# Kernel optimization log

Measured on AMD Instinct MI355X. Metric: run time of the kernel, lower is better.

Reference implementation:

```python
import jax, jax.numpy as jnp
import numpy as np

N_NODES = 50000
N_EDGES = 1600000
D = 128
N_GRAPHS = 512


def _glorot(key, shape):
    fan_in, fan_out = shape[1], shape[0]
    lim = float(np.sqrt(6.0 / (fan_in + fan_out)))
    return jax.random.uniform(key, shape, jnp.float32, -lim, lim)


def setup_inputs() -> dict:
    key = jax.random.key(0)
    ks = jax.random.split(key, 16)
    inp = {
        "x": jax.random.normal(ks[0], (N_NODES, D), jnp.float32),
        "edge_index": jax.random.randint(ks[1], (2, N_EDGES), 0, N_NODES, jnp.int64),
        "batch": jnp.sort(jax.random.randint(ks[2], (N_NODES,), 0, N_GRAPHS, jnp.int64)),
    }
    # 3 SAGEConv layers: W_l (neighbor path, with bias), W_r (root path, no bias)
    for l in range(3):
        inp[f"Wl{l}"] = _glorot(ks[3 + 3 * l], (D, D))
        inp[f"b{l}"] = jnp.zeros((D,), jnp.float32)
        inp[f"Wr{l}"] = _glorot(ks[4 + 3 * l], (D, D))
    inp["fc_w"] = _glorot(ks[14], (1, D))
    inp["fc_b"] = jnp.zeros((1,), jnp.float32)
    return inp


def _sage_layer(x, src, dst, Wl, b, Wr):
    # mean aggregation of source features at destination nodes
    deg = jax.ops.segment_sum(jnp.ones((src.shape[0],), x.dtype), dst, num_segments=N_NODES)
    agg = jax.ops.segment_sum(x[src], dst, num_segments=N_NODES)  # [N, D] gather+scatter
    agg = agg / jnp.clip(deg, 1.0)[:, None]
    return agg @ Wl.T + b + x @ Wr.T


def reference(x, edge_index, batch, Wl0, b0, Wr0, Wl1, b1, Wr1, Wl2, b2, Wr2, fc_w, fc_b):
    src, dst = edge_index[0], edge_index[1]
    for Wl, b, Wr in ((Wl0, b0, Wr0), (Wl1, b1, Wr1), (Wl2, b2, Wr2)):
        x = jax.nn.relu(_sage_layer(x, src, dst, Wl, b, Wr))  # dropout p=0 -> identity
    # global mean pool per graph
    cnt = jax.ops.segment_sum(jnp.ones((x.shape[0],), x.dtype), batch, num_segments=N_GRAPHS)
    pooled = jax.ops.segment_sum(x, batch, num_segments=N_GRAPHS) / jnp.clip(cnt, 1.0)[:, None]
    return pooled @ fc_w.T + fc_b
```

## Files before the change

### kernel.cpp

```cpp
#include <hip/hip_runtime.h>

#define N_NODES  50000
#define N_EDGES  1600000
#define DIM      128
#define N_GRAPHS 512
#define SCAN_BLOCK 1024
#define NB1   196
#define B1    256
#define CHUNK 6250
#define BH_N  (NB1 * B1)
#define BH_BLK ((BH_N + SCAN_BLOCK - 1) / SCAN_BLOCK)

typedef unsigned int uint_t;
typedef unsigned short ushort_t;
typedef __attribute__((ext_vector_type(8))) short bf16x8;
typedef __attribute__((ext_vector_type(4))) float f32x4;

__device__ inline uint_t bf_rne(float f) {
    uint_t u = __float_as_uint(f);
    return (u + 0x7fffu + ((u >> 16) & 1u)) >> 16;
}

__device__ inline void bf_split(float f, uint_t& h, uint_t& l) {
    h = bf_rne(f);
    float hf = __uint_as_float(h << 16);
    l = bf_rne(f - hf);
}

__global__ __launch_bounds__(256) void p1_count(const int* __restrict__ dst,
                                                int* __restrict__ bh) {
    __shared__ int hist[NB1];
    int b = blockIdx.x, t = threadIdx.x;
    for (int i = t; i < NB1; i += 256) hist[i] = 0;
    __syncthreads();
    int base = b * CHUNK;
    for (int i = t; i < CHUNK; i += 256)
        atomicAdd(&hist[dst[base + i] >> 8], 1);
    __syncthreads();
    for (int i = t; i < NB1; i += 256) bh[i * B1 + b] = hist[i];
}

__global__ void block_reduce_n(const int* __restrict__ in, int* __restrict__ bsum, int n) {
    __shared__ int red[256];
    int b = blockIdx.x, t = threadIdx.x;
    int base = b * SCAN_BLOCK;
    int s = 0;
    for (int i = t; i < SCAN_BLOCK; i += 256) {
        int idx = base + i;
        s += (idx < n) ? in[idx] : 0;
    }
    red[t] = s; __syncthreads();
    for (int off = 128; off; off >>= 1) {
        if (t < off) red[t] += red[t + off];
        __syncthreads();
    }
    if (t == 0) bsum[b] = red[0];
}

__global__ void scan_tops_n(const int* __restrict__ bsum, int* __restrict__ bofs, int nblk) {
    if (threadIdx.x == 0) {
        int acc = 0;
        for (int i = 0; i < nblk; i++) { bofs[i] = acc; acc += bsum[i]; }
    }
}

__global__ void block_scan_n(const int* __restrict__ in, const int* __restrict__ bofs,
                             int* __restrict__ ofs, int n) {
    __shared__ int tmp[SCAN_BLOCK];
    int b = blockIdx.x, t = threadIdx.x;
    int i = b * SCAN_BLOCK + t;
    tmp[t] = (i < n) ? in[i] : 0;
    __syncthreads();
    for (int off = 1; off < SCAN_BLOCK; off <<= 1) {
        int add = (t >= off) ? tmp[t - off] : 0;
        __syncthreads();
        tmp[t] += add;
        __syncthreads();
    }
    if (i < n) ofs[i + 1] = tmp[t] + bofs[b];
    if (i == 0) ofs[0] = 0;
}

__global__ __launch_bounds__(256) void p1_scatter(const int* __restrict__ src,
                                                  const int* __restrict__ dst,
                                                  const int* __restrict__ bhofs,
                                                  uint_t* __restrict__ ebuf1) {
    __shared__ int cur[NB1];
    int b = blockIdx.x, t = threadIdx.x;
    for (int i = t; i < NB1; i += 256) cur[i] = bhofs[i * B1 + b];
    __syncthreads();
    int base = b * CHUNK;
    for (int i = t; i < CHUNK; i += 256) {
        int d = dst[base + i];
        int pos = atomicAdd(&cur[d >> 8], 1);
        ebuf1[pos] = (uint_t)src[base + i] | ((uint_t)(d & 255) << 16);
    }
}

__global__ __launch_bounds__(256) void p2_sort(const uint_t* __restrict__ ebuf1,
                                               const int* __restrict__ bhofs,
                                               int* __restrict__ row_start,
                                               int* __restrict__ ebuf) {
    __shared__ int hist[256];
    __shared__ int scn[256];
    __shared__ int cur[256];
    int k = blockIdx.x, t = threadIdx.x;
    int s = bhofs[k * B1];
    int e = (k == NB1 - 1) ? N_EDGES : bhofs[(k + 1) * B1];
    hist[t] = 0;
    __syncthreads();
    for (int i = s + t; i < e; i += 256)
        atomicAdd(&hist[(ebuf1[i] >> 16) & 255], 1);
    __syncthreads();
    int v = hist[t];
    scn[t] = v;
    __syncthreads();
    for (int off = 1; off < 256; off <<= 1) {
        int add = (t >= off) ? scn[t - off] : 0;
        __syncthreads();
        scn[t] += add;
        __syncthreads();
    }
    int ex = scn[t] - v;
    int node = k * 256 + t;
    if (node < N_NODES) row_start[node] = s + ex;
    if (k == NB1 - 1 && t == 0) row_start[N_NODES] = N_EDGES;
    cur[t] = s + ex;
    __syncthreads();
    for (int i = s + t; i < e; i += 256) {
        uint_t p = ebuf1[i];
        int pos = atomicAdd(&cur[(p >> 16) & 255], 1);
        ebuf[pos] = (int)(p & 0xffffu);
    }
}

__global__ void xsplit(const float* __restrict__ x, ushort_t* __restrict__ xh,
                       ushort_t* __restrict__ xl) {
    int i = blockIdx.x * 256 + threadIdx.x;
    if (i < (N_NODES * DIM) / 4) {
        float4 v = ((const float4*)x)[i];
        uint_t h0,h1,h2,h3,l0,l1,l2,l3;
        bf_split(v.x,h0,l0); bf_split(v.y,h1,l1); bf_split(v.z,h2,l2); bf_split(v.w,h3,l3);
        uint2 ho; ho.x = h0 | (h1 << 16); ho.y = h2 | (h3 << 16);
        uint2 lo; lo.x = l0 | (l1 << 16); lo.y = l2 | (l3 << 16);
        ((uint2*)xh)[i] = ho;
        ((uint2*)xl)[i] = lo;
    }
}

__global__ void wsplit6(const float* w0, const float* w1, const float* w2,
                        const float* w3, const float* w4, const float* w5,
                        ushort_t* __restrict__ whi) {
    int i = blockIdx.x * 256 + threadIdx.x;
    if (i < 6 * 16384) {
        int ws = i >> 14, off = i & 16383;
        const float* w = (ws == 0) ? w0 : (ws == 1) ? w1 : (ws == 2) ? w2
                       : (ws == 3) ? w3 : (ws == 4) ? w4 : w5;
        whi[i] = (ushort_t)bf_rne(w[off]);
    }
}

__global__ __launch_bounds__(256) void agg_kernel(const ushort_t* __restrict__ xb,
                                                  const int* __restrict__ row_start,
                                                  const int* __restrict__ ebuf,
                                                  ushort_t* __restrict__ agg_hi,
                                                  ushort_t* __restrict__ agg_lo) {
    int node = blockIdx.x * 4 + (threadIdx.x >> 6);
    if (node >= N_NODES) return;
    int lane = threadIdx.x & 63;
    int grp = lane >> 4, fl = lane & 15;
    int s = row_start[node], e = row_start[node + 1];
    float a0=0.f,a1=0.f,a2=0.f,a3=0.f,a4=0.f,a5=0.f,a6=0.f,a7=0.f;
    const uint4* x8 = (const uint4*)xb;
    for (int i = s; i < e; i += 64) {
        int nloc = e - i; if (nloc > 64) nloc = 64;
        int src_l = (i + lane < e) ? ebuf[i + lane] : 0;
        int jmax = (nloc + 3) & ~3;
        #pragma unroll 2
        for (int j = 0; j < jmax; j += 4) {
            int slot = j + grp;
            int src = __shfl(src_l, slot & 63, 64);
            if (slot < nloc) {
                uint4 v = x8[(size_t)src * 16 + fl];
                a0 += __uint_as_float(v.x << 16);
                a1 += __uint_as_float(v.x & 0xffff0000u);
                a2 += __uint_as_float(v.y << 16);
                a3 += __uint_as_float(v.y & 0xffff0000u);
                a4 += __uint_as_float(v.z << 16);
                a5 += __uint_as_float(v.z & 0xffff0000u);
                a6 += __uint_as_float(v.w << 16);
                a7 += __uint_as_float(v.w & 0xffff0000u);
            }
        }
    }
    a0 += __shfl_xor(a0, 16, 64); a0 += __shfl_xor(a0, 32, 64);
    a1 += __shfl_xor(a1, 16, 64); a1 += __shfl_xor(a1, 32, 64);
    a2 += __shfl_xor(a2, 16, 64); a2 += __shfl_xor(a2, 32, 64);
    a3 += __shfl_xor(a3, 16, 64); a3 += __shfl_xor(a3, 32, 64);
    a4 += __shfl_xor(a4, 16, 64); a4 += __shfl_xor(a4, 32, 64);
    a5 += __shfl_xor(a5, 16, 64); a5 += __shfl_xor(a5, 32, 64);
    a6 += __shfl_xor(a6, 16, 64); a6 += __shfl_xor(a6, 32, 64);
    a7 += __shfl_xor(a7, 16, 64); a7 += __shfl_xor(a7, 32, 64);
    if (grp == 0) {
        float inv = (e > s) ? 1.0f / (float)(e - s) : 0.0f;
        float v[8] = {a0*inv,a1*inv,a2*inv,a3*inv,a4*inv,a5*inv,a6*inv,a7*inv};
        uint_t h[8], l[8];
        #pragma unroll
        for (int k = 0; k < 8; k++) bf_split(v[k], h[k], l[k]);
        uint4 ho, lo;
        ho.x = h[0] | (h[1] << 16); ho.y = h[2] | (h[3] << 16);
        ho.z = h[4] | (h[5] << 16); ho.w = h[6] | (h[7] << 16);
        lo.x = l[0] | (l[1] << 16); lo.y = l[2] | (l[3] << 16);
        lo.z = l[4] | (l[5] << 16); lo.w = l[6] | (l[7] << 16);
        ((uint4*)agg_hi)[(size_t)node * 16 + fl] = ho;
        ((uint4*)agg_lo)[(size_t)node * 16 + fl] = lo;
    }
}

__global__ __launch_bounds__(256, 2) void sage_gemm_mfma(
        const ushort_t* __restrict__ agg_hi, const ushort_t* __restrict__ agg_lo,
        const ushort_t* __restrict__ x_hi,   const ushort_t* __restrict__ x_lo,
        const ushort_t* __restrict__ wl_hi,  const ushort_t* __restrict__ wr_hi,
        const float* __restrict__ bias,
        ushort_t* __restrict__ out_hi, ushort_t* __restrict__ out_lo, int nrows) {
    __shared__ ushort_t whi_s[2][16384];
    int t = threadIdx.x;
    for (int i = t; i < 4096; i += 256) {
        int a = i >> 11, rem = i & 2047, row = rem >> 4, ch = rem & 15;
        int sw = ch ^ (row & 7);
        const ushort_t* srcp = a ? wr_hi : wl_hi;
        uint4 v = *(const uint4*)(srcp + row * DIM + ch * 8);
        *(uint4*)((char*)&whi_s[a][0] + row * 256 + sw * 16) = v;
    }
    __syncthreads();

    int wave = t >> 6, lane = t & 63;
    int ml = lane & 15, quad = lane >> 4;
    int m0 = blockIdx.x * 64 + wave * 16;
    int row = m0 + ml;
    int rowc = (row < nrows) ? row : (nrows - 1);
    size_t abase = (size_t)rowc * DIM + quad * 8;

    f32x4 acc[8];
    #pragma unroll
    for (int i = 0; i < 8; i++) acc[i] = (f32x4)0.f;

    #pragma unroll
    for (int kc = 0; kc < DIM; kc += 32) {
        bf16x8 Aah = *(const bf16x8*)(agg_hi + abase + kc);
        bf16x8 Aal = *(const bf16x8*)(agg_lo + abase + kc);
        bf16x8 Axh = *(const bf16x8*)(x_hi   + abase + kc);
        bf16x8 Axl = *(const bf16x8*)(x_lo   + abase + kc);
        int kch = (kc >> 3) + quad;
        int sw16 = (kch ^ (ml & 7)) * 16;
        #pragma unroll
        for (int n0 = 0; n0 < 8; n0++) {
            int nrow = n0 * 16 + ml;
            bf16x8 b_lh = *(const bf16x8*)((const char*)&whi_s[0][0] + nrow * 256 + sw16);
            bf16x8 b_rh = *(const bf16x8*)((const char*)&whi_s[1][0] + nrow * 256 + sw16);
            f32x4 c = acc[n0];
            c = __builtin_amdgcn_mfma_f32_16x16x32_bf16(Aah, b_lh, c, 0, 0, 0);
            c = __builtin_amdgcn_mfma_f32_16x16x32_bf16(Aal, b_lh, c, 0, 0, 0);
            c = __builtin_amdgcn_mfma_f32_16x16x32_bf16(Axh, b_rh, c, 0, 0, 0);
            c = __builtin_amdgcn_mfma_f32_16x16x32_bf16(Axl, b_rh, c, 0, 0, 0);
            acc[n0] = c;
        }
    }

    #pragma unroll
    for (int n0 = 0; n0 < 8; n0++) {
        int col = n0 * 16 + ml;
        float bv = bias[col];
        #pragma unroll
        for (int r = 0; r < 4; r++) {
            int orow = m0 + quad * 4 + r;
            if (orow < nrows) {
                float v = fmaxf(acc[n0][r] + bv, 0.f);
                uint_t h, l;
                bf_split(v, h, l);
                out_hi[(size_t)orow * DIM + col] = (ushort_t)h;
                out_lo[(size_t)orow * DIM + col] = (ushort_t)l;
            }
        }
    }
}

__global__ void graph_bounds(const int* __restrict__ batch, int* __restrict__ gstart) {
    int i = blockIdx.x * 256 + threadIdx.x;
    if (i < N_NODES) {
        int b = batch[i];
        int prev = (i == 0) ? -1 : batch[i - 1];
        for (int g = prev + 1; g <= b; g++) gstart[g] = i;
        if (i == 0) {
            int last = batch[N_NODES - 1];
            for (int g = last + 1; g <= N_GRAPHS; g++) gstart[g] = N_NODES;
        }
    }
}

__global__ __launch_bounds__(256) void pool_fc(const ushort_t* __restrict__ x_hi,
                                               const ushort_t* __restrict__ x_lo,
                                               const int* __restrict__ gstart,
                                               const float* __restrict__ fc_w,
                                               const float* __restrict__ fc_b,
                                               float* __restrict__ out) {
    int g = blockIdx.x * 4 + (threadIdx.x >> 6);
    if (g >= N_GRAPHS) return;
    int lane = threadIdx.x & 63;
    int s = gstart[g], e = gstart[g + 1];
    float ax = 0.f, ay = 0.f;
    const uint_t* xh = (const uint_t*)x_hi;
    const uint_t* xl = (const uint_t*)x_lo;
    for (int i = s; i < e; i++) {
        uint_t h = xh[(size_t)i * 64 + lane];
        uint_t l = xl[(size_t)i * 64 + lane];
        ax += __uint_as_float(h << 16) + __uint_as_float(l << 16);
        ay += __uint_as_float(h & 0xffff0000u) + __uint_as_float(l & 0xffff0000u);
    }
    float inv = (e > s) ? 1.0f / (float)(e - s) : 0.0f;
    const float2* w2 = (const float2*)fc_w;
    float2 w = w2[lane];
    float sres = (ax * w.x + ay * w.y) * inv;
    for (int off = 32; off; off >>= 1) sres += __shfl_down(sres, off, 64);
    if (lane == 0) out[g] = sres + fc_b[0];
}

extern "C" void kernel_launch(void* const* d_in, const int* in_sizes, int n_in,
                              void* d_out, int out_size, void* d_ws, size_t ws_size,
                              hipStream_t stream) {
    const float* x     = (const float*)d_in[0];
    const int*   ei    = (const int*)d_in[1];
    const int*   batch = (const int*)d_in[2];
    const float* Wl[3] = {(const float*)d_in[3], (const float*)d_in[6], (const float*)d_in[9]};
    const float* bb[3] = {(const float*)d_in[4], (const float*)d_in[7], (const float*)d_in[10]};
    const float* Wr[3] = {(const float*)d_in[5], (const float*)d_in[8], (const float*)d_in[11]};
    const float* fc_w  = (const float*)d_in[12];
    const float* fc_b  = (const float*)d_in[13];
    float* out = (float*)d_out;

    char* p = (char*)d_ws;
    auto alloc = [&](size_t bytes) { char* r = p; p += (bytes + 255) & ~255ull; return r; };
    int* bh        = (int*)alloc((size_t)BH_N * 4);
    int* bhofs     = (int*)alloc((size_t)(BH_N + 1) * 4);
    int* bsum      = (int*)alloc((size_t)BH_BLK * 4);
    int* bofs      = (int*)alloc((size_t)BH_BLK * 4);
    uint_t* ebuf1  = (uint_t*)alloc((size_t)N_EDGES * 4);
    int* ebuf      = (int*)alloc((size_t)N_EDGES * 4);
    int* row_start = (int*)alloc((size_t)(N_NODES + 1) * 4);
    int* gstart    = (int*)alloc((size_t)(N_GRAPHS + 1) * 4);
    const size_t FB = (size_t)N_NODES * DIM * 2;
    ushort_t* agg_hi = (ushort_t*)alloc(FB);
    ushort_t* agg_lo = (ushort_t*)alloc(FB);
    ushort_t* fh[3]  = {(ushort_t*)alloc(FB), (ushort_t*)alloc(FB), (ushort_t*)alloc(FB)};
    ushort_t* fl_[3] = {(ushort_t*)alloc(FB), (ushort_t*)alloc(FB), (ushort_t*)alloc(FB)};
    ushort_t* whi    = (ushort_t*)alloc((size_t)6 * 16384 * 2);

    const int* src = ei;
    const int* dst = ei + N_EDGES;

    p1_count<<<B1, 256, 0, stream>>>(dst, bh);
    block_reduce_n<<<BH_BLK, 256, 0, stream>>>(bh, bsum, BH_N);
    scan_tops_n<<<1, 64, 0, stream>>>(bsum, bofs, BH_BLK);
    block_scan_n<<<BH_BLK, SCAN_BLOCK, 0, stream>>>(bh, bofs, bhofs, BH_N);
    p1_scatter<<<B1, 256, 0, stream>>>(src, dst, bhofs, ebuf1);
    p2_sort<<<NB1, 256, 0, stream>>>(ebuf1, bhofs, row_start, ebuf);
    graph_bounds<<<(N_NODES + 255) / 256, 256, 0, stream>>>(batch, gstart);
    xsplit<<<(N_NODES * DIM / 4 + 255) / 256, 256, 0, stream>>>(x, fh[0], fl_[0]);
    wsplit6<<<(6 * 16384 + 255) / 256, 256, 0, stream>>>(Wl[0], Wr[0], Wl[1], Wr[1], Wl[2], Wr[2], whi);

    int inb = 0;
    for (int l = 0; l < 3; l++) {
        int outb = (l == 0) ? 1 : (l == 1) ? 2 : 1;
        agg_kernel<<<(N_NODES + 3) / 4, 256, 0, stream>>>(fh[inb], row_start, ebuf, agg_hi, agg_lo);
        sage_gemm_mfma<<<(N_NODES + 63) / 64, 256, 0, stream>>>(
            agg_hi, agg_lo, fh[inb], fl_[inb],
            whi + (size_t)(2 * l) * 16384, whi + (size_t)(2 * l + 1) * 16384,
            bb[l], fh[outb], fl_[outb], N_NODES);
        inb = outb;
    }
    pool_fc<<<(N_GRAPHS + 3) / 4, 256, 0, stream>>>(fh[inb], fl_[inb], gstart, fc_w, fc_b, out);
}
```

Baseline: 452.1 us.

## Split aggregation across feature chunks and fuse prep kernels into one launch

The aggregation kernel now splits the 128 features into four 32-feature chunks via blockIdx.y. Each wavefront handles eight edges at once with 8-byte loads instead of four edges with 16-byte loads, which gives more parallelism per node and fewer registers per thread. The price is that each chunk's block rereads the edge list and row bounds. The three preprocessing kernels (x split, weight split, graph bounds) are also merged into one launch to cut launch overhead.

```diff
diff --git a/kernel.cpp b/kernel.cpp
--- a/kernel.cpp
+++ b/kernel.cpp
@@ -10,6 +10,9 @@
 #define CHUNK 6250
 #define BH_N  (NB1 * B1)
 #define BH_BLK ((BH_N + SCAN_BLOCK - 1) / SCAN_BLOCK)
+#define XS_BLOCKS 6250
+#define WS_BLOCKS 384
+#define GB_BLOCKS 196
 
 typedef unsigned int uint_t;
 typedef unsigned short ushort_t;
@@ -134,10 +137,15 @@
     }
 }
 
-__global__ void xsplit(const float* __restrict__ x, ushort_t* __restrict__ xh,
-                       ushort_t* __restrict__ xl) {
-    int i = blockIdx.x * 256 + threadIdx.x;
-    if (i < (N_NODES * DIM) / 4) {
+__global__ __launch_bounds__(256) void prep_kernel(
+        const float* __restrict__ x, ushort_t* __restrict__ xh, ushort_t* __restrict__ xl,
+        const float* w0, const float* w1, const float* w2,
+        const float* w3, const float* w4, const float* w5,
+        ushort_t* __restrict__ whi,
+        const int* __restrict__ batch, int* __restrict__ gstart) {
+    int b = blockIdx.x, t = threadIdx.x;
+    if (b < XS_BLOCKS) {
+        int i = b * 256 + t;
         float4 v = ((const float4*)x)[i];
         uint_t h0,h1,h2,h3,l0,l1,l2,l3;
         bf_split(v.x,h0,l0); bf_split(v.y,h1,l1); bf_split(v.z,h2,l2); bf_split(v.w,h3,l3);
@@ -145,18 +153,23 @@
         uint2 lo; lo.x = l0 | (l1 << 16); lo.y = l2 | (l3 << 16);
         ((uint2*)xh)[i] = ho;
         ((uint2*)xl)[i] = lo;
-    }
-}
-
-__global__ void wsplit6(const float* w0, const float* w1, const float* w2,
-                        const float* w3, const float* w4, const float* w5,
-                        ushort_t* __restrict__ whi) {
-    int i = blockIdx.x * 256 + threadIdx.x;
-    if (i < 6 * 16384) {
+    } else if (b < XS_BLOCKS + WS_BLOCKS) {
+        int i = (b - XS_BLOCKS) * 256 + t;
         int ws = i >> 14, off = i & 16383;
         const float* w = (ws == 0) ? w0 : (ws == 1) ? w1 : (ws == 2) ? w2
                        : (ws == 3) ? w3 : (ws == 4) ? w4 : w5;
         whi[i] = (ushort_t)bf_rne(w[off]);
+    } else {
+        int i = (b - XS_BLOCKS - WS_BLOCKS) * 256 + t;
+        if (i < N_NODES) {
+            int bb = batch[i];
+            int prev = (i == 0) ? -1 : batch[i - 1];
+            for (int g = prev + 1; g <= bb; g++) gstart[g] = i;
+            if (i == 0) {
+                int last = batch[N_NODES - 1];
+                for (int g = last + 1; g <= N_GRAPHS; g++) gstart[g] = N_NODES;
+            }
+        }
     }
 }
 
@@ -166,54 +179,48 @@
                                                   ushort_t* __restrict__ agg_hi,
                                                   ushort_t* __restrict__ agg_lo) {
     int node = blockIdx.x * 4 + (threadIdx.x >> 6);
-    if (node >= N_NODES) return;
+    int chunk = blockIdx.y;
     int lane = threadIdx.x & 63;
-    int grp = lane >> 4, fl = lane & 15;
+    int grp = lane >> 3, fl = lane & 7;
     int s = row_start[node], e = row_start[node + 1];
-    float a0=0.f,a1=0.f,a2=0.f,a3=0.f,a4=0.f,a5=0.f,a6=0.f,a7=0.f;
-    const uint4* x8 = (const uint4*)xb;
+    float2 a0, a1;
+    a0.x = a0.y = a1.x = a1.y = 0.f;
+    const uint2* x2 = (const uint2*)xb;
+    int cofs = chunk * 8 + fl;
     for (int i = s; i < e; i += 64) {
         int nloc = e - i; if (nloc > 64) nloc = 64;
         int src_l = (i + lane < e) ? ebuf[i + lane] : 0;
-        int jmax = (nloc + 3) & ~3;
-        #pragma unroll 2
-        for (int j = 0; j < jmax; j += 4) {
-            int slot = j + grp;
-            int src = __shfl(src_l, slot & 63, 64);
+        int jmax = (nloc + 7) >> 3;
+        #pragma unroll 4
+        for (int j = 0; j < jmax; j++) {
+            int slot = j * 8 + grp;
+            int src = __shfl(src_l, slot, 64);
             if (slot < nloc) {
-                uint4 v = x8[(size_t)src * 16 + fl];
-                a0 += __uint_as_float(v.x << 16);
-                a1 += __uint_as_float(v.x & 0xffff0000u);
-                a2 += __uint_as_float(v.y << 16);
-                a3 += __uint_as_float(v.y & 0xffff0000u);
-                a4 += __uint_as_float(v.z << 16);
-                a5 += __uint_as_float(v.z & 0xffff0000u);
-                a6 += __uint_as_float(v.w << 16);
-                a7 += __uint_as_float(v.w & 0xffff0000u);
+                uint2 v = x2[(size_t)src * 32 + cofs];
+                a0.x += __uint_as_float(v.x << 16);
+                a0.y += __uint_as_float(v.x & 0xffff0000u);
+                a1.x += __uint_as_float(v.y << 16);
+                a1.y += __uint_as_float(v.y & 0xffff0000u);
             }
         }
     }
-    a0 += __shfl_xor(a0, 16, 64); a0 += __shfl_xor(a0, 32, 64);
-    a1 += __shfl_xor(a1, 16, 64); a1 += __shfl_xor(a1, 32, 64);
-    a2 += __shfl_xor(a2, 16, 64); a2 += __shfl_xor(a2, 32, 64);
-    a3 += __shfl_xor(a3, 16, 64); a3 += __shfl_xor(a3, 32, 64);
-    a4 += __shfl_xor(a4, 16, 64); a4 += __shfl_xor(a4, 32, 64);
-    a5 += __shfl_xor(a5, 16, 64); a5 += __shfl_xor(a5, 32, 64);
-    a6 += __shfl_xor(a6, 16, 64); a6 += __shfl_xor(a6, 32, 64);
-    a7 += __shfl_xor(a7, 16, 64); a7 += __shfl_xor(a7, 32, 64);
+    #pragma unroll
+    for (int off = 8; off <= 32; off <<= 1) {
+        a0.x += __shfl_xor(a0.x, off, 64);
+        a0.y += __shfl_xor(a0.y, off, 64);
+        a1.x += __shfl_xor(a1.x, off, 64);
+        a1.y += __shfl_xor(a1.y, off, 64);
+    }
     if (grp == 0) {
         float inv = (e > s) ? 1.0f / (float)(e - s) : 0.0f;
-        float v[8] = {a0*inv,a1*inv,a2*inv,a3*inv,a4*inv,a5*inv,a6*inv,a7*inv};
-        uint_t h[8], l[8];
-        #pragma unroll
-        for (int k = 0; k < 8; k++) bf_split(v[k], h[k], l[k]);
-        uint4 ho, lo;
-        ho.x = h[0] | (h[1] << 16); ho.y = h[2] | (h[3] << 16);
-        ho.z = h[4] | (h[5] << 16); ho.w = h[6] | (h[7] << 16);
-        lo.x = l[0] | (l[1] << 16); lo.y = l[2] | (l[3] << 16);
-        lo.z = l[4] | (l[5] << 16); lo.w = l[6] | (l[7] << 16);
-        ((uint4*)agg_hi)[(size_t)node * 16 + fl] = ho;
-        ((uint4*)agg_lo)[(size_t)node * 16 + fl] = lo;
+        float v0 = a0.x * inv, v1 = a0.y * inv, v2 = a1.x * inv, v3 = a1.y * inv;
+        uint_t h0,h1,h2,h3,l0,l1,l2,l3;
+        bf_split(v0,h0,l0); bf_split(v1,h1,l1); bf_split(v2,h2,l2); bf_split(v3,h3,l3);
+        uint2 ho; ho.x = h0 | (h1 << 16); ho.y = h2 | (h3 << 16);
+        uint2 lo; lo.x = l0 | (l1 << 16); lo.y = l2 | (l3 << 16);
+        int widx = node * 32 + cofs;
+        ((uint2*)agg_hi)[widx] = ho;
+        ((uint2*)agg_lo)[widx] = lo;
     }
 }
 
@@ -285,19 +292,6 @@
     }
 }
 
-__global__ void graph_bounds(const int* __restrict__ batch, int* __restrict__ gstart) {
-    int i = blockIdx.x * 256 + threadIdx.x;
-    if (i < N_NODES) {
-        int b = batch[i];
-        int prev = (i == 0) ? -1 : batch[i - 1];
-        for (int g = prev + 1; g <= b; g++) gstart[g] = i;
-        if (i == 0) {
-            int last = batch[N_NODES - 1];
-            for (int g = last + 1; g <= N_GRAPHS; g++) gstart[g] = N_NODES;
-        }
-    }
-}
-
 __global__ __launch_bounds__(256) void pool_fc(const ushort_t* __restrict__ x_hi,
                                                const ushort_t* __restrict__ x_lo,
                                                const int* __restrict__ gstart,
@@ -364,14 +358,13 @@
     block_scan_n<<<BH_BLK, SCAN_BLOCK, 0, stream>>>(bh, bofs, bhofs, BH_N);
     p1_scatter<<<B1, 256, 0, stream>>>(src, dst, bhofs, ebuf1);
     p2_sort<<<NB1, 256, 0, stream>>>(ebuf1, bhofs, row_start, ebuf);
-    graph_bounds<<<(N_NODES + 255) / 256, 256, 0, stream>>>(batch, gstart);
-    xsplit<<<(N_NODES * DIM / 4 + 255) / 256, 256, 0, stream>>>(x, fh[0], fl_[0]);
-    wsplit6<<<(6 * 16384 + 255) / 256, 256, 0, stream>>>(Wl[0], Wr[0], Wl[1], Wr[1], Wl[2], Wr[2], whi);
+    prep_kernel<<<XS_BLOCKS + WS_BLOCKS + GB_BLOCKS, 256, 0, stream>>>(
+        x, fh[0], fl_[0], Wl[0], Wr[0], Wl[1], Wr[1], Wl[2], Wr[2], whi, batch, gstart);
 
     int inb = 0;
     for (int l = 0; l < 3; l++) {
         int outb = (l == 0) ? 1 : (l == 1) ? 2 : 1;
-        agg_kernel<<<(N_NODES + 3) / 4, 256, 0, stream>>>(fh[inb], row_start, ebuf, agg_hi, agg_lo);
+        agg_kernel<<<dim3(N_NODES / 4, 4), 256, 0, stream>>>(fh[inb], row_start, ebuf, agg_hi, agg_lo);
         sage_gemm_mfma<<<(N_NODES + 63) / 64, 256, 0, stream>>>(
             agg_hi, agg_lo, fh[inb], fl_[inb],
             whi + (size_t)(2 * l) * 16384, whi + (size_t)(2 * l + 1) * 16384,
```

After: 575.0 us. 1.27x slower.
